# Kernel optimization log

Hardware: AMD Instinct MI355X
Metric: run time of the kernel (lower is better)

## Reference

```python
import jax, jax.numpy as jnp
import numpy as np

B, T, C, H = 2, 2048, 1024, 4
D = C // H
STRIDES = [1, 3, 7, 13]  # spiral_strides[:n_head]
SCALE = 1.0 / float(np.sqrt(D))


def _build_mask():
    """Static [H, T, T] bool mask: spiral positions intersected with causal.
    Replicates: positions = set((i+offset)%T for offset in range(-T//2, T//2, stride)),
    then keep only p <= i."""
    m = np.zeros((H, T, T), dtype=bool)
    i = np.arange(T)
    causal = (np.arange(T)[None, :] <= i[:, None])
    for h in range(H):
        s = STRIDES[h % len(STRIDES)]
        off = np.arange(-(T // 2), T // 2, s)
        pos = (i[:, None] + off[None, :]) % T  # [T, n_off]
        mh = np.zeros((T, T), dtype=bool)
        mh[np.repeat(i, len(off)), pos.ravel()] = True  # set semantics (dupes ok)
        m[h] = mh & causal
    return jnp.asarray(m)

MASK = _build_mask()  # [H, T, T]


def setup_inputs() -> dict:
    ks = jax.random.split(jax.random.key(0), 4)
    s = 0.02
    return {
        "x": jax.random.normal(ks[0], (B, T, C), jnp.float32),
        "Wqk": jax.random.normal(ks[1], (C, C), jnp.float32) * s,
        "bqk": jnp.zeros((C,), jnp.float32),
        "Wv": jax.random.normal(ks[2], (C, C), jnp.float32) * s,
        "bv": jnp.zeros((C,), jnp.float32),
        "Wo": jax.random.normal(ks[3], (C, C), jnp.float32) * s,
        "bo": jnp.zeros((C,), jnp.float32),
    }


def reference(x, Wqk, bqk, Wv, bv, Wo, bo):
    qk = x @ Wqk.T + bqk                                   # [B,T,C]; q == k in source
    q = qk.reshape(B, T, H, D).transpose(0, 2, 1, 3)       # [B,H,T,D]
    v = (x @ Wv.T + bv).reshape(B, T, H, D).transpose(0, 2, 1, 3)
    scores = jnp.einsum('bhid,bhjd->bhij', q, q) * SCALE   # [B,H,T,T]
    NEG = jnp.float32(-1e30)
    logits = jnp.where(MASK[None], scores, NEG)
    w = jax.nn.softmax(logits, axis=-1)
    # Rows with no causal spiral position stay all-zero (matches torch scatter behavior)
    w = jnp.where(MASK[None], w, jnp.float32(0.0))
    out = jnp.einsum('bhij,bhjd->bhid', w, v)              # [B,H,T,D]
    out = out.transpose(0, 2, 1, 3).reshape(B, T, C)
    return out @ Wo.T + bo
```

## Files before the change

### kernel.cpp

```cpp
#include <hip/hip_runtime.h>
#include <cstdint>
#include <cstddef>

typedef unsigned short u16;
typedef uint32_t u32;
typedef __bf16 bf16x8 __attribute__((ext_vector_type(8)));
typedef float f32x4 __attribute__((ext_vector_type(4)));
typedef float f32x16 __attribute__((ext_vector_type(16)));

typedef __attribute__((address_space(1))) void gvoid;
typedef __attribute__((address_space(3))) void lvoid;

__device__ __forceinline__ void g2l16(const void* g, void* l) {
    __builtin_amdgcn_global_load_lds((gvoid*)g, (lvoid*)l, 16, 0, 0);
}

__device__ __forceinline__ u16 f2bf(float f) {
    union { float f; uint32_t u; } v;
    v.f = f;
    uint32_t r = (v.u + 0x7FFFu + ((v.u >> 16) & 1u)) >> 16;
    return (u16)r;
}

__device__ const int T_h[24]  = {0, 1,1,1, 2,2,2,2,2,2,2, 3,3,3,3,3,3,3,3,3,3,3,3,3};
__device__ const int T_g[24]  = {0, 0,1,2, 0,1,2,3,4,5,6, 0,1,2,3,4,5,6,7,8,9,10,11,12};
__device__ const int T_qt[24] = {0, 64,86,108, 130,140,150,160,170,180,190,
                                 200,205,210,215,220,225,230,235,240,245,250,255,260};
__device__ const int T_LQ[24] = {2048, 683,683,682, 293,293,293,293,292,292,292,
                                 158,158,158,158,158,158,158,157,157,157,157,157,157};
__device__ const int T_ktB[24]= {0, 64,86,108, 140,150,160,170,180,190,130,
                                 245,250,255,260,200,205,210,215,220,225,230,235,240};
__device__ const int T_LkB[24]= {2048, 683,683,682, 293,293,293,292,292,292,293,
                                 157,157,157,157,158,158,158,158,158,158,158,157,157};
__device__ const int T_cB[24] = {1, -341,-341,-341, -146,-146,-146,-146,-146,-146,-145,
                                 -79,-79,-79,-79,-78,-78,-78,-78,-78,-78,-78,-78,-78};
__device__ const int T_ktA[24]= {0, 108,64,86, 180,190,130,140,150,160,170,
                                 215,220,225,230,235,240,245,250,255,260,200,205,210};
__device__ const int T_LkA[24]= {0, 682,683,683, 292,292,293,293,293,293,292,
                                 158,158,158,158,157,157,157,157,157,157,158,158,158};
__device__ const int T_cA[24] = {0, -342,-341,-341, -147,-147,-146,-146,-146,-146,-146,
                                 -79,-79,-79,-79,-79,-79,-79,-79,-79,-79,-78,-78,-78};
__device__ const int T_dA[24] = {0, 0,1,1, 0,0,1,1,1,1,1, 0,0,0,0,0,0,0,0,0,0,1,1,1};
__device__ const int T_nc[24] = {16, 6,6,6, 3,3,3,3,3,3,3, 2,2,2,2,2,2,2,2,2,2,2,2,2};

__device__ __forceinline__ void col_geom(int p, int c, int& ntB, int& tA0, int& nt) {
    const int LQ = T_LQ[p];
    const int Mc = c << 7;
    int mmax = Mc + 128; if (mmax > LQ) mmax = LQ; mmax -= 1;
    int jB = mmax + T_cB[p];
    if (jB < 0) jB = 0;
    if (jB > T_LkB[p]) jB = T_LkB[p];
    ntB = (jB + 31) >> 5;
    int jlo = Mc + T_cA[p]; if (jlo < 0) jlo = 0;
    int jhi = mmax + T_dA[p];
    if (jhi > T_LkA[p]) jhi = T_LkA[p];
    tA0 = jlo >> 5;
    int ntA = 0;
    if (jhi > jlo) ntA = ((jhi + 31) >> 5) - tA0;
    nt = ntB + ntA;
}

__device__ __forceinline__ u16* partO_addr(u16* lo, u16* hi, int slot) {
    return (slot < 128) ? (lo + (size_t)slot * 32768) : (hi + (size_t)(slot - 128) * 32768);
}
__device__ __forceinline__ const u16* partO_addr_c(const u16* lo, const u16* hi, int slot) {
    return (slot < 128) ? (lo + (size_t)slot * 32768) : (hi + (size_t)(slot - 128) * 32768);
}

__global__ __launch_bounds__(256)
void cvt_kernel(const float* __restrict__ x, const float* __restrict__ wqk,
                const float* __restrict__ wv, const float* __restrict__ wo,
                u16* __restrict__ out) {
    int i = (blockIdx.x * 256 + threadIdx.x) * 4;
    const float* src;
    int off;
    if (i < 4194304)      { src = x;   off = 0; }
    else if (i < 5242880) { src = wqk; off = 4194304; }
    else if (i < 6291456) { src = wv;  off = 5242880; }
    else                  { src = wo;  off = 6291456; }
    float4 v = *(const float4*)(src + (i - off));
    ushort4 o;
    o.x = f2bf(v.x); o.y = f2bf(v.y); o.z = f2bf(v.z); o.w = f2bf(v.w);
    *(ushort4*)(out + i) = o;
}

__global__ __launch_bounds__(256)
void gemm_qkv(const u16* __restrict__ A, const u16* __restrict__ Bq, const u16* __restrict__ Bv,
              const float* __restrict__ bq, const float* __restrict__ bv,
              u16* __restrict__ qkb, u16* __restrict__ vb) {
    __shared__ __align__(16) u16 As[2][4096], Bqs[2][2048], Bvs[2][2048];
    const int bid = blockIdx.x;
    const int m0 = (bid >> 4) * 128;
    const int n0 = (bid & 15) * 64;
    const int t = threadIdx.x;
    const int lane = t & 63;
    const int wid = t >> 6;
    const int wr = wid >> 1, wc = wid & 1;
    const int l15 = lane & 15, l4 = lane >> 4;

    f32x4 aq[4][2] = {}, av[4][2] = {};

    auto stage = [&](int buf, int kt) {
        const int kbase = kt * 32;
#pragma unroll
        for (int c2 = 0; c2 < 2; ++c2) {
            const int pp = c2 * 4096 + t * 16;
            g2l16(A + (size_t)(m0 + (pp >> 6)) * 1024 + kbase + ((pp & 63) >> 1), (char*)As[buf] + pp);
        }
        const int pb = t * 16;
        const int rb = pb >> 6, kb = (pb & 63) >> 1;
        g2l16(Bq + (size_t)(n0 + rb) * 1024 + kbase + kb, (char*)Bqs[buf] + pb);
        g2l16(Bv + (size_t)(n0 + rb) * 1024 + kbase + kb, (char*)Bvs[buf] + pb);
    };

    stage(0, 0);
    asm volatile("s_waitcnt vmcnt(0)" ::: "memory");
    __syncthreads();

    int cur = 0;
    for (int kt = 0; kt < 32; ++kt) {
        if (kt + 1 < 32) stage(cur ^ 1, kt + 1);
        bf16x8 af[4], bfq[2], bfv[2];
#pragma unroll
        for (int mi = 0; mi < 4; ++mi)
            af[mi] = *(const bf16x8*)((const char*)As[cur] + (wr * 64 + mi * 16 + l15) * 64 + l4 * 16);
#pragma unroll
        for (int ni = 0; ni < 2; ++ni) {
            bfq[ni] = *(const bf16x8*)((const char*)Bqs[cur] + (wc * 32 + ni * 16 + l15) * 64 + l4 * 16);
            bfv[ni] = *(const bf16x8*)((const char*)Bvs[cur] + (wc * 32 + ni * 16 + l15) * 64 + l4 * 16);
        }
#pragma unroll
        for (int mi = 0; mi < 4; ++mi)
#pragma unroll
            for (int ni = 0; ni < 2; ++ni) {
                aq[mi][ni] = __builtin_amdgcn_mfma_f32_16x16x32_bf16(af[mi], bfq[ni], aq[mi][ni], 0, 0, 0);
                av[mi][ni] = __builtin_amdgcn_mfma_f32_16x16x32_bf16(af[mi], bfv[ni], av[mi][ni], 0, 0, 0);
            }
        asm volatile("s_waitcnt vmcnt(0)" ::: "memory");
        __syncthreads();
        cur ^= 1;
    }

    const int mbase = m0 + wr * 64 + l4 * 4;
    const int nbase = n0 + wc * 32 + l15;
#pragma unroll
    for (int ni = 0; ni < 2; ++ni) {
        const int n = nbase + ni * 16;
        const float bq_ = bq[n];
        const float bv_ = bv[n];
#pragma unroll
        for (int mi = 0; mi < 4; ++mi) {
            const int mrow = mbase + mi * 16;
#pragma unroll
            for (int r = 0; r < 4; ++r) {
                qkb[(size_t)(mrow + r) * 1024 + n] = f2bf(aq[mi][ni][r] + bq_);
                vb [(size_t)(mrow + r) * 1024 + n] = f2bf(av[mi][ni][r] + bv_);
            }
        }
    }
}

__device__ __forceinline__ void tile_decode(int tt, int& h, int& cls, int& jt, int& LK) {
    if (tt < 64)       { h = 0; cls = 0;               jt = tt;              LK = 2048; }
    else if (tt < 130) { h = 1; cls = (tt - 64) / 22;  jt = (tt - 64) % 22;  LK = (cls < 2) ? 683 : 682; }
    else if (tt < 200) { h = 2; cls = (tt - 130) / 10; jt = (tt - 130) % 10; LK = (cls < 4) ? 293 : 292; }
    else               { h = 3; cls = (tt - 200) / 5;  jt = (tt - 200) % 5;  LK = (cls < 7) ? 158 : 157; }
}

__global__ __launch_bounds__(256)
void repack_v(const u16* __restrict__ vb, u16* __restrict__ vpack) {
    __shared__ __align__(16) unsigned char sm[16384];
    const int bid = blockIdx.x;
    const int b = bid & 1;
    const int tt = bid >> 1;
    int h, cls, jt, LK;
    tile_decode(tt, h, cls, jt, LK);
    const int s = (h == 0) ? 1 : (h == 1) ? 3 : (h == 2) ? 7 : 13;
    const int j0 = jt * 32;
    int nval = LK - j0; if (nval > 32) nval = 32;
    const int t = threadIdx.x;

#pragma unroll
    for (int i2 = 0; i2 < 4; ++i2) {
        const int p = i2 * 4096 + t * 16;
        const int j = p >> 9;
        const int cb = (p & 511) ^ ((j & 31) << 4);
        const int jj = (j < nval) ? j : (nval - 1);
        const int tok = cls + (j0 + jj) * s;
        g2l16(vb + (size_t)((b * 2048 + tok) * 1024 + h * 256) + (cb >> 1), sm + p);
    }
    asm volatile("s_waitcnt vmcnt(0)" ::: "memory");
    __syncthreads();
    if (nval < 32) {
        const int pb = nval * 512;
        for (int off = pb + t * 16; off < 16384; off += 4096) {
            uint4 z; z.x = 0; z.y = 0; z.z = 0; z.w = 0;
            *(uint4*)(sm + off) = z;
        }
        __syncthreads();
    }
    const size_t tb = (size_t)(b * 265 + tt) * 8192;
#pragma unroll
    for (int i2 = 0; i2 < 4; ++i2) {
        const int o = (i2 * 256 + t) * 8;
        const int slot2 = o >> 9;
        const int idx = (o >> 3) & 63;
        const int jb = (slot2 >> 3) * 16 + (idx >> 5) * 8;
        const int d = (slot2 & 7) * 32 + (idx & 31);
        u32 wpk[4];
#pragma unroll
        for (int e2 = 0; e2 < 4; ++e2) {
            const int j1 = jb + e2 * 2, j2 = j1 + 1;
            const u16 a0 = *(const u16*)(sm + j1 * 512 + (((d >> 3) ^ (j1 & 31)) << 4) + (d & 7) * 2);
            const u16 a1 = *(const u16*)(sm + j2 * 512 + (((d >> 3) ^ (j2 & 31)) << 4) + (d & 7) * 2);
            wpk[e2] = (u32)a0 | ((u32)a1 << 16);
        }
        uint4 pk; pk.x = wpk[0]; pk.y = wpk[1]; pk.z = wpk[2]; pk.w = wpk[3];
        *(uint4*)(vpack + tb + o) = pk;
    }
}

__global__ __launch_bounds__(256)
void repack_k(const u16* __restrict__ qkb, u16* __restrict__ kpack) {
    __shared__ __align__(16) unsigned char sm[16384];
    const int bid = blockIdx.x;
    const int b = bid & 1;
    const int tt = bid >> 1;
    int h, cls, jt, LK;
    tile_decode(tt, h, cls, jt, LK);
    const int s = (h == 0) ? 1 : (h == 1) ? 3 : (h == 2) ? 7 : 13;
    const int j0 = jt * 32;
    int nval = LK - j0; if (nval > 32) nval = 32;
    const int t = threadIdx.x;

#pragma unroll
    for (int i2 = 0; i2 < 4; ++i2) {
        const int p = i2 * 4096 + t * 16;
        const int j = p >> 9;
        const int cb = (p & 511) ^ ((j & 31) << 4);
        const int jj = (j < nval) ? j : (nval - 1);
        const int tok = cls + (j0 + jj) * s;
        g2l16(qkb + (size_t)((b * 2048 + tok) * 1024 + h * 256) + (cb >> 1), sm + p);
    }
    asm volatile("s_waitcnt vmcnt(0)" ::: "memory");
    __syncthreads();
    const size_t tb = (size_t)(b * 265 + tt) * 8192;
#pragma unroll
    for (int i2 = 0; i2 < 4; ++i2) {
        const int o = (i2 * 256 + t) * 8;
        const int dc = o >> 9;
        const int idx = (o >> 3) & 63;
        const int j = idx & 31;
        const int d0 = dc * 16 + (idx >> 5) * 8;
        const uint4 pk = *(const uint4*)(sm + j * 512 + ((d0 * 2) ^ ((j & 31) << 4)));
        *(uint4*)(kpack + tb + o) = pk;
    }
}

__global__ __launch_bounds__(256, 2)
void attn_kernel(const u16* __restrict__ kpack, const u16* __restrict__ vpack,
                 u16* __restrict__ attnb, u16* __restrict__ partLo, u16* __restrict__ partHi,
                 float* __restrict__ mlbuf) {
    __shared__ __align__(16) unsigned char sm[65536];
    static constexpr int CGc[24] = {0,16,22,28,34,37,40,43,46,49,52,55,
                                    57,59,61,63,65,67,69,71,73,75,77,79};
    static constexpr int EXc[24] = {0,56,64,72,80,82,84,86,88,90,92,94,
                                    94,94,94,94,94,94,94,94,94,94,94,94};
    static constexpr int Tpc[24] = {72,14,14,14,5,5,5,5,5,5,5,2,2,2,2,2,2,2,2,2,2,2,2,2};

    const int bid = blockIdx.x;
    const int xcd = bid & 7, slot = bid >> 3;
    const int b = xcd & 1, quad = xcd >> 1;
    int hsel, hcb;
    if (quad <= 1) {
        if (slot < 36)      { hsel = 0; hcb = quad * 36 + slot; }
        else if (slot < 49) { hsel = 3; hcb = quad * 13 + (slot - 36); }
        else return;
    } else if (quad == 2) {
        if (slot >= 42) return;
        hsel = 1; hcb = slot;
    } else {
        if (slot >= 35) return;
        hsel = 2; hcb = slot;
    }
    int p = (hsel == 0) ? 0 : (hsel == 1) ? 1 : (hsel == 2) ? 4 : 11;
    int rb = hcb;
    while (rb >= Tpc[p]) { rb -= Tpc[p]; ++p; }
    int colg = CGc[p], exb = EXc[p];

    const int LQ = T_LQ[p];
    const int cB = T_cB[p], cA = T_cA[p], dA = T_dA[p];
    const int LKB = T_LkB[p], LKA = T_LkA[p];
    const int ktB = T_ktB[p], ktA = T_ktA[p];
    const int h = T_h[p], g = T_g[p], nc = T_nc[p], qt0 = T_qt[p];
    const int s = (h == 0) ? 1 : (h == 1) ? 3 : (h == 2) ? 7 : 13;

    int col = 0, chunk = 0, ntB = 0, tA0 = 0, nt = 0;
    for (int c = nc - 1; c >= 0; --c) {
        const int Mc = c << 7;
        int mmax = Mc + 128; if (mmax > LQ) mmax = LQ; mmax -= 1;
        int jB = mmax + cB; if (jB < 0) jB = 0; if (jB > LKB) jB = LKB;
        const int nb = (jB + 31) >> 5;
        int jlo = Mc + cA; if (jlo < 0) jlo = 0;
        int jhi = mmax + dA; if (jhi > LKA) jhi = LKA;
        const int ta = jlo >> 5;
        const int na = (jhi > jlo) ? (((jhi + 31) >> 5) - ta) : 0;
        const int n = nb + na;
        const int nch2 = (n + 7) >> 3;
        if (rb < nch2) { col = c; chunk = rb; ntB = nb; tA0 = ta; nt = n; break; }
        rb -= nch2; ++colg; exb += nch2 - 1;
    }
    const int nch = (nt + 7) >> 3;
    const int PBi = b * 265;

    const int t = threadIdx.x;
    const int w = t >> 6;
    const int l = t & 63;
    const int l31 = l & 31, h5 = l >> 5;
    const int m = (col << 7) + (w << 5) + l31;
    const float c2 = 0.09016844f;
    const int lane16 = l * 16;

    bf16x8 qf[16];
    {
        const u16* qb = kpack + (size_t)(PBi + qt0 + col * 4 + w) * 8192 + l * 8;
#pragma unroll
        for (int dc = 0; dc < 16; ++dc)
            qf[dc] = *(const bf16x8*)(qb + dc * 512);
    }

    auto tileof = [&](int tv) -> int {
        return (tv < ntB) ? (ktB + tv) : (ktA + tA0 + (tv - ntB));
    };
    auto stage = [&](int tv, int buf) {
        const size_t tb = (size_t)(PBi + tileof(tv)) * 8192;
        unsigned char* Kd = sm + buf * 32768;
        unsigned char* Vd = Kd + 16384;
#pragma unroll
        for (int i2 = 0; i2 < 4; ++i2) {
            const int off = i2 * 4096 + t * 16;
            g2l16(kpack + tb + (off >> 1), Kd + off);
            g2l16(vpack + tb + (off >> 1), Vd + off);
        }
    };

    const int tt0 = chunk * 8;
    int tt1 = tt0 + 8; if (tt1 > nt) tt1 = nt;

    f32x16 o[8] = {};
    float mrun = -3.0e38f, lrun = 0.0f;

    stage(tt0, 0);
    asm volatile("s_waitcnt vmcnt(0)" ::: "memory");
    __syncthreads();

    int buf = 0;
    for (int tv = tt0; tv < tt1; ++tv) {
        if (tv + 1 < tt1) stage(tv + 1, buf ^ 1);

        int j0, lo, hi;
        if (tv < ntB) { j0 = tv << 5; lo = -100000; hi = cB; }
        else { const int ta = tA0 + tv - ntB; j0 = ta << 5; lo = cA; hi = dA; }

        const unsigned char* Kb = sm + buf * 32768;
        const unsigned char* Vb = Kb + 16384;

        f32x16 sacc = {};
#pragma unroll
        for (int dc = 0; dc < 16; ++dc) {
            const bf16x8 kf = *(const bf16x8*)(Kb + dc * 1024 + lane16);
            sacc = __builtin_amdgcn_mfma_f32_32x32x16_bf16(kf, qf[dc], sacc, 0, 0, 0);
        }

        const int ebase = j0 - m;
        float tmax = -3.0e38f;
#pragma unroll
        for (int r = 0; r < 16; ++r) {
            const int km = (r & 3) + 8 * (r >> 2) + 4 * h5;
            const int e = ebase + km;
            const bool ok = (e >= lo) && (e < hi);
            sacc[r] = ok ? sacc[r] : -3.0e38f;
            tmax = fmaxf(tmax, sacc[r]);
        }
        tmax = fmaxf(tmax, __shfl_xor(tmax, 32, 64));
        if (!__all(tmax <= mrun + 8.0f)) {
            const float mnew = fmaxf(mrun, tmax);
            const float fsc = __builtin_amdgcn_exp2f((mrun - mnew) * c2);
            lrun *= fsc;
#pragma unroll
            for (int ch = 0; ch < 8; ++ch)
#pragma unroll
                for (int r = 0; r < 16; ++r)
                    o[ch][r] *= fsc;
            mrun = mnew;
        }
        float psum = 0.0f;
#pragma unroll
        for (int r = 0; r < 16; ++r) {
            const float pv = (sacc[r] > -1.0e37f) ? __builtin_amdgcn_exp2f((sacc[r] - mrun) * c2) : 0.0f;
            sacc[r] = pv;
            psum += pv;
        }
        lrun += psum;

        uint32_t w0, w1, w2, w3, w4, w5, w6, w7;
        asm("v_cvt_pk_bf16_f32 %0,%1,%2" : "=v"(w0) : "v"(sacc[0]),  "v"(sacc[1]));
        asm("v_cvt_pk_bf16_f32 %0,%1,%2" : "=v"(w1) : "v"(sacc[2]),  "v"(sacc[3]));
        asm("v_cvt_pk_bf16_f32 %0,%1,%2" : "=v"(w2) : "v"(sacc[4]),  "v"(sacc[5]));
        asm("v_cvt_pk_bf16_f32 %0,%1,%2" : "=v"(w3) : "v"(sacc[6]),  "v"(sacc[7]));
        asm("v_cvt_pk_bf16_f32 %0,%1,%2" : "=v"(w4) : "v"(sacc[8]),  "v"(sacc[9]));
        asm("v_cvt_pk_bf16_f32 %0,%1,%2" : "=v"(w5) : "v"(sacc[10]), "v"(sacc[11]));
        asm("v_cvt_pk_bf16_f32 %0,%1,%2" : "=v"(w6) : "v"(sacc[12]), "v"(sacc[13]));
        asm("v_cvt_pk_bf16_f32 %0,%1,%2" : "=v"(w7) : "v"(sacc[14]), "v"(sacc[15]));
        asm("v_permlane32_swap_b32 %0, %1" : "+v"(w0), "+v"(w2));
        asm("v_permlane32_swap_b32 %0, %1" : "+v"(w1), "+v"(w3));
        asm("v_permlane32_swap_b32 %0, %1" : "+v"(w4), "+v"(w6));
        asm("v_permlane32_swap_b32 %0, %1" : "+v"(w5), "+v"(w7));
        union { uint32_t u[4]; bf16x8 v; } p0u, p1u;
        p0u.u[0] = w0; p0u.u[1] = w1; p0u.u[2] = w2; p0u.u[3] = w3;
        p1u.u[0] = w4; p1u.u[1] = w5; p1u.u[2] = w6; p1u.u[3] = w7;

#pragma unroll
        for (int kk = 0; kk < 2; ++kk) {
            const bf16x8 pf = kk ? p1u.v : p0u.v;
#pragma unroll
            for (int ch = 0; ch < 8; ++ch) {
                const bf16x8 vf = *(const bf16x8*)(Vb + (kk * 8 + ch) * 1024 + lane16);
                o[ch] = __builtin_amdgcn_mfma_f32_32x32x16_bf16(vf, pf, o[ch], 0, 0, 0);
            }
        }

        asm volatile("s_waitcnt vmcnt(0)" ::: "memory");
        __syncthreads();
        buf ^= 1;
    }

    lrun += __shfl_xor(lrun, 32, 64);

    float scale = 1.0f;
    u16* ab;
    const int qm = (w << 5) + l31;
    if (nch == 1) {
        scale = (lrun > 0.0f) ? 1.0f / lrun : 0.0f;
        ab = attnb + ((size_t)(b * 2048 + g + m * s)) * 1024 + h * 256;
    } else {
        if (h5 == 0 && m < LQ) {
            const int colid = b * 81 + colg;
            mlbuf[(size_t)((colid * 8 + chunk) * 256) + qm * 2]     = mrun;
            mlbuf[(size_t)((colid * 8 + chunk) * 256) + qm * 2 + 1] = lrun;
        }
        if (chunk == 0)
            ab = attnb + ((size_t)(b * 2048 + g + m * s)) * 1024 + h * 256;
        else
            ab = partO_addr(partLo, partHi, b * 94 + exb + chunk - 1) + (size_t)qm * 256;
    }

    if (m < LQ) {
#pragma unroll
        for (int ch = 0; ch < 8; ++ch) {
#pragma unroll
            for (int g2 = 0; g2 < 4; ++g2) {
                ushort4 wv4;
                wv4.x = f2bf(o[ch][g2 * 4 + 0] * scale);
                wv4.y = f2bf(o[ch][g2 * 4 + 1] * scale);
                wv4.z = f2bf(o[ch][g2 * 4 + 2] * scale);
                wv4.w = f2bf(o[ch][g2 * 4 + 3] * scale);
                *(ushort4*)(ab + ch * 32 + 8 * g2 + 4 * h5) = wv4;
            }
        }
    }
}

__global__ __launch_bounds__(256)
void combine_kernel(const u16* __restrict__ partLo, const u16* __restrict__ partHi,
                    const float* __restrict__ mlbuf, u16* __restrict__ attnb) {
    static constexpr int MCc[24] = {0,14,18,22,26,28,30,32,34,36,38,40,
                                    40,40,40,40,40,40,40,40,40,40,40,40};
    static constexpr int CGc[24] = {0,16,22,28,34,37,40,43,46,49,52,55,
                                    57,59,61,63,65,67,69,71,73,75,77,79};
    static constexpr int EXc[24] = {0,56,64,72,80,82,84,86,88,90,92,94,
                                    94,94,94,94,94,94,94,94,94,94,94,94};
    const int b = blockIdx.x & 1;
    int rb = blockIdx.x >> 1;
    int p = 0, base = 0, colg = 0, exb = 0;
#pragma unroll
    for (int i = 1; i < 24; ++i)
        if (rb >= MCc[i]) { p = i; base = MCc[i]; colg = CGc[i]; exb = EXc[i]; }
    rb -= base;

    int col = 0, nch = 0;
    for (int c = T_nc[p] - 1; c >= 0; --c) {
        int nb, ta, n;
        col_geom(p, c, nb, ta, n);
        const int nc2 = (n + 7) >> 3;
        if (nc2 > 1) {
            if (rb == 0) { col = c; nch = nc2; break; }
            --rb;
        }
        ++colg; exb += nc2 - 1;
    }
    const int h = T_h[p], g = T_g[p];
    const int s = (h == 0) ? 1 : (h == 1) ? 3 : (h == 2) ? 7 : 13;
    const int LQ = T_LQ[p];
    const int colid = b * 81 + colg;
    const float c2 = 0.09016844f;

    const int t = threadIdx.x;
    const int q = t >> 1, dpart = (t & 1) * 128;
    const int m = (col << 7) + q;

    float mj[8], lj[8];
#pragma unroll
    for (int j5 = 0; j5 < 8; ++j5) {
        if (j5 < nch) {
            mj[j5] = mlbuf[(size_t)((colid * 8 + j5) * 256) + q * 2];
            lj[j5] = mlbuf[(size_t)((colid * 8 + j5) * 256) + q * 2 + 1];
        } else { mj[j5] = -3.0e38f; lj[j5] = 0.0f; }
    }
    float M = -3.0e38f;
#pragma unroll
    for (int j5 = 0; j5 < 8; ++j5) if (j5 < nch) M = fmaxf(M, mj[j5]);
    float L = 0.0f, al[8];
#pragma unroll
    for (int j5 = 0; j5 < 8; ++j5) {
        al[j5] = (j5 < nch) ? __builtin_amdgcn_exp2f((mj[j5] - M) * c2) : 0.0f;
        L += lj[j5] * al[j5];
    }
    const float inv = (L > 0.0f) ? 1.0f / L : 0.0f;
#pragma unroll
    for (int j5 = 0; j5 < 8; ++j5) al[j5] *= inv;

    u16* dst = attnb + ((size_t)(b * 2048 + g + m * s)) * 1024 + h * 256 + dpart;

    for (int ss = 0; ss < 4; ++ss) {
        float acc32[32];
#pragma unroll
        for (int e = 0; e < 32; ++e) acc32[e] = 0.0f;
#pragma unroll
        for (int j5 = 0; j5 < 8; ++j5) {
            if (j5 >= nch) continue;
            const u16* src = (j5 == 0)
                ? (dst + ss * 32)
                : (partO_addr_c(partLo, partHi, b * 94 + exb + j5 - 1) + (size_t)q * 256 + dpart + ss * 32);
            const float sc = al[j5];
#pragma unroll
            for (int w4 = 0; w4 < 4; ++w4) {
                const uint4 pk = *(const uint4*)(src + w4 * 8);
                const u32 ww[4] = { pk.x, pk.y, pk.z, pk.w };
#pragma unroll
                for (int e = 0; e < 4; ++e) {
                    union { u32 u; float f; } lo2, hi2;
                    lo2.u = ww[e] << 16;
                    hi2.u = ww[e] & 0xffff0000u;
                    acc32[w4 * 8 + e * 2]     += sc * lo2.f;
                    acc32[w4 * 8 + e * 2 + 1] += sc * hi2.f;
                }
            }
        }
        if (m < LQ) {
#pragma unroll
            for (int w4 = 0; w4 < 4; ++w4) {
                uint4 pk;
                pk.x = (u32)f2bf(acc32[w4 * 8 + 0]) | ((u32)f2bf(acc32[w4 * 8 + 1]) << 16);
                pk.y = (u32)f2bf(acc32[w4 * 8 + 2]) | ((u32)f2bf(acc32[w4 * 8 + 3]) << 16);
                pk.z = (u32)f2bf(acc32[w4 * 8 + 4]) | ((u32)f2bf(acc32[w4 * 8 + 5]) << 16);
                pk.w = (u32)f2bf(acc32[w4 * 8 + 6]) | ((u32)f2bf(acc32[w4 * 8 + 7]) << 16);
                *(uint4*)(dst + ss * 32 + w4 * 8) = pk;
            }
        }
    }
}

__global__ __launch_bounds__(256)
void gemm_out(const u16* __restrict__ A, const u16* __restrict__ Bw,
              const float* __restrict__ bias, float* __restrict__ outp) {
    __shared__ __align__(16) u16 As[2][4096], Bs[2][2048];
    const int bid = blockIdx.x;
    const int m0 = (bid >> 4) * 128;
    const int n0 = (bid & 15) * 64;
    const int t = threadIdx.x;
    const int lane = t & 63;
    const int wid = t >> 6;
    const int wr = wid >> 1, wc = wid & 1;
    const int l15 = lane & 15, l4 = lane >> 4;

    f32x4 acc[4][2] = {};

    auto stage = [&](int buf, int kt) {
        const int kbase = kt * 32;
#pragma unroll
        for (int c2 = 0; c2 < 2; ++c2) {
            const int pp = c2 * 4096 + t * 16;
            g2l16(A + (size_t)(m0 + (pp >> 6)) * 1024 + kbase + ((pp & 63) >> 1), (char*)As[buf] + pp);
        }
        const int pb = t * 16;
        g2l16(Bw + (size_t)(n0 + (pb >> 6)) * 1024 + kbase + ((pb & 63) >> 1), (char*)Bs[buf] + pb);
    };

    stage(0, 0);
    asm volatile("s_waitcnt vmcnt(0)" ::: "memory");
    __syncthreads();

    int cur = 0;
    for (int kt = 0; kt < 32; ++kt) {
        if (kt + 1 < 32) stage(cur ^ 1, kt + 1);
        bf16x8 af[4], bfr[2];
#pragma unroll
        for (int mi = 0; mi < 4; ++mi)
            af[mi] = *(const bf16x8*)((const char*)As[cur] + (wr * 64 + mi * 16 + l15) * 64 + l4 * 16);
#pragma unroll
        for (int ni = 0; ni < 2; ++ni)
            bfr[ni] = *(const bf16x8*)((const char*)Bs[cur] + (wc * 32 + ni * 16 + l15) * 64 + l4 * 16);
#pragma unroll
        for (int mi = 0; mi < 4; ++mi)
#pragma unroll
            for (int ni = 0; ni < 2; ++ni)
                acc[mi][ni] = __builtin_amdgcn_mfma_f32_16x16x32_bf16(af[mi], bfr[ni], acc[mi][ni], 0, 0, 0);
        asm volatile("s_waitcnt vmcnt(0)" ::: "memory");
        __syncthreads();
        cur ^= 1;
    }

    const int mbase = m0 + wr * 64 + l4 * 4;
    const int nbase = n0 + wc * 32 + l15;
#pragma unroll
    for (int ni = 0; ni < 2; ++ni) {
        const int n = nbase + ni * 16;
        const float bv = bias[n];
#pragma unroll
        for (int mi = 0; mi < 4; ++mi) {
            const int mrow = mbase + mi * 16;
#pragma unroll
            for (int r = 0; r < 4; ++r)
                outp[(size_t)(mrow + r) * 1024 + n] = acc[mi][ni][r] + bv;
        }
    }
}

extern "C" void kernel_launch(void* const* d_in, const int* in_sizes, int n_in,
                              void* d_out, int out_size, void* d_ws, size_t ws_size,
                              hipStream_t stream) {
    const float* x   = (const float*)d_in[0];
    const float* Wqk = (const float*)d_in[1];
    const float* bqk = (const float*)d_in[2];
    const float* Wv  = (const float*)d_in[3];
    const float* bv  = (const float*)d_in[4];
    const float* Wo  = (const float*)d_in[5];
    const float* bo  = (const float*)d_in[6];
    float* out = (float*)d_out;

    u16* ws     = (u16*)d_ws;
    u16* xb     = ws;
    u16* wqkb   = ws + 4194304;
    u16* wvb    = ws + 5242880;
    u16* wob    = ws + 6291456;
    u16* qkb    = ws + 7340032;
    u16* vb     = ws + 11534336;
    u16* kpack  = ws + 11534336;
    u16* vpack  = ws + 15876096;
    u16* attnb  = ws;
    u16* partLo = ws + 7340032;
    u16* partHi = ws + 4194304;
    float* mlbuf = (float*)d_out;

    cvt_kernel<<<7168, 256, 0, stream>>>(x, Wqk, Wv, Wo, ws);
    gemm_qkv<<<512, 256, 0, stream>>>(xb, wqkb, wvb, bqk, bv, qkb, vb);
    repack_v<<<530, 256, 0, stream>>>(vb, vpack);
    repack_k<<<530, 256, 0, stream>>>(qkb, kpack);
    attn_kernel<<<392, 256, 0, stream>>>(kpack, vpack, attnb, partLo, partHi, mlbuf);
    combine_kernel<<<80, 256, 0, stream>>>(partLo, partHi, mlbuf, attnb);
    gemm_out<<<512, 256, 0, stream>>>(attnb, wob, bo, out);
}
```

Before: 132.7 us.

## Fuse K/V repack kernels and add MFMA priority hints and occupancy bounds

Merges the separate repack_v and repack_k kernels into one repack_kv launch that gathers both K and V tiles into a 32KB LDS buffer, removing a kernel launch and a duplicate index computation. Because kpack previously aliased the vb buffer, it moves kpack and vpack to new workspace offsets, which needs a larger workspace. It also wraps the MFMA loops in the GEMMs and the attention kernel with s_setprio raises, and adds a min-blocks-per-CU hint of 3 to both GEMMs, which may constrain register allocation.

New measurement: 123.5 us. -6.9%, faster.

```diff
diff --git a/kernel.cpp b/kernel.cpp
--- a/kernel.cpp
+++ b/kernel.cpp
@@ -84,7 +84,7 @@
     *(ushort4*)(out + i) = o;
 }
 
-__global__ __launch_bounds__(256)
+__global__ __launch_bounds__(256, 3)
 void gemm_qkv(const u16* __restrict__ A, const u16* __restrict__ Bq, const u16* __restrict__ Bv,
               const float* __restrict__ bq, const float* __restrict__ bv,
               u16* __restrict__ qkb, u16* __restrict__ vb) {
@@ -129,6 +129,7 @@
             bfq[ni] = *(const bf16x8*)((const char*)Bqs[cur] + (wc * 32 + ni * 16 + l15) * 64 + l4 * 16);
             bfv[ni] = *(const bf16x8*)((const char*)Bvs[cur] + (wc * 32 + ni * 16 + l15) * 64 + l4 * 16);
         }
+        __builtin_amdgcn_s_setprio(1);
 #pragma unroll
         for (int mi = 0; mi < 4; ++mi)
 #pragma unroll
@@ -136,6 +137,7 @@
                 aq[mi][ni] = __builtin_amdgcn_mfma_f32_16x16x32_bf16(af[mi], bfq[ni], aq[mi][ni], 0, 0, 0);
                 av[mi][ni] = __builtin_amdgcn_mfma_f32_16x16x32_bf16(af[mi], bfv[ni], av[mi][ni], 0, 0, 0);
             }
+        __builtin_amdgcn_s_setprio(0);
         asm volatile("s_waitcnt vmcnt(0)" ::: "memory");
         __syncthreads();
         cur ^= 1;
@@ -168,8 +170,9 @@
 }
 
 __global__ __launch_bounds__(256)
-void repack_v(const u16* __restrict__ vb, u16* __restrict__ vpack) {
-    __shared__ __align__(16) unsigned char sm[16384];
+void repack_kv(const u16* __restrict__ qkb, const u16* __restrict__ vb,
+               u16* __restrict__ kpack, u16* __restrict__ vpack) {
+    __shared__ __align__(16) unsigned char sm[32768];
     const int bid = blockIdx.x;
     const int b = bid & 1;
     const int tt = bid >> 1;
@@ -186,64 +189,20 @@
         const int j = p >> 9;
         const int cb = (p & 511) ^ ((j & 31) << 4);
         const int jj = (j < nval) ? j : (nval - 1);
-        const int tok = cls + (j0 + jj) * s;
-        g2l16(vb + (size_t)((b * 2048 + tok) * 1024 + h * 256) + (cb >> 1), sm + p);
+        const size_t gofs = (size_t)((b * 2048 + cls + (j0 + jj) * s) * 1024 + h * 256) + (cb >> 1);
+        g2l16(qkb + gofs, sm + p);
+        g2l16(vb  + gofs, sm + 16384 + p);
     }
     asm volatile("s_waitcnt vmcnt(0)" ::: "memory");
     __syncthreads();
     if (nval < 32) {
-        const int pb = nval * 512;
-        for (int off = pb + t * 16; off < 16384; off += 4096) {
+        const int pb = 16384 + nval * 512;
+        for (int off = pb + t * 16; off < 32768; off += 4096) {
             uint4 z; z.x = 0; z.y = 0; z.z = 0; z.w = 0;
             *(uint4*)(sm + off) = z;
         }
         __syncthreads();
     }
-    const size_t tb = (size_t)(b * 265 + tt) * 8192;
-#pragma unroll
-    for (int i2 = 0; i2 < 4; ++i2) {
-        const int o = (i2 * 256 + t) * 8;
-        const int slot2 = o >> 9;
-        const int idx = (o >> 3) & 63;
-        const int jb = (slot2 >> 3) * 16 + (idx >> 5) * 8;
-        const int d = (slot2 & 7) * 32 + (idx & 31);
-        u32 wpk[4];
-#pragma unroll
-        for (int e2 = 0; e2 < 4; ++e2) {
-            const int j1 = jb + e2 * 2, j2 = j1 + 1;
-            const u16 a0 = *(const u16*)(sm + j1 * 512 + (((d >> 3) ^ (j1 & 31)) << 4) + (d & 7) * 2);
-            const u16 a1 = *(const u16*)(sm + j2 * 512 + (((d >> 3) ^ (j2 & 31)) << 4) + (d & 7) * 2);
-            wpk[e2] = (u32)a0 | ((u32)a1 << 16);
-        }
-        uint4 pk; pk.x = wpk[0]; pk.y = wpk[1]; pk.z = wpk[2]; pk.w = wpk[3];
-        *(uint4*)(vpack + tb + o) = pk;
-    }
-}
-
-__global__ __launch_bounds__(256)
-void repack_k(const u16* __restrict__ qkb, u16* __restrict__ kpack) {
-    __shared__ __align__(16) unsigned char sm[16384];
-    const int bid = blockIdx.x;
-    const int b = bid & 1;
-    const int tt = bid >> 1;
-    int h, cls, jt, LK;
-    tile_decode(tt, h, cls, jt, LK);
-    const int s = (h == 0) ? 1 : (h == 1) ? 3 : (h == 2) ? 7 : 13;
-    const int j0 = jt * 32;
-    int nval = LK - j0; if (nval > 32) nval = 32;
-    const int t = threadIdx.x;
-
-#pragma unroll
-    for (int i2 = 0; i2 < 4; ++i2) {
-        const int p = i2 * 4096 + t * 16;
-        const int j = p >> 9;
-        const int cb = (p & 511) ^ ((j & 31) << 4);
-        const int jj = (j < nval) ? j : (nval - 1);
-        const int tok = cls + (j0 + jj) * s;
-        g2l16(qkb + (size_t)((b * 2048 + tok) * 1024 + h * 256) + (cb >> 1), sm + p);
-    }
-    asm volatile("s_waitcnt vmcnt(0)" ::: "memory");
-    __syncthreads();
     const size_t tb = (size_t)(b * 265 + tt) * 8192;
 #pragma unroll
     for (int i2 = 0; i2 < 4; ++i2) {
@@ -254,6 +213,24 @@
         const int d0 = dc * 16 + (idx >> 5) * 8;
         const uint4 pk = *(const uint4*)(sm + j * 512 + ((d0 * 2) ^ ((j & 31) << 4)));
         *(uint4*)(kpack + tb + o) = pk;
+    }
+#pragma unroll
+    for (int i2 = 0; i2 < 4; ++i2) {
+        const int o = (i2 * 256 + t) * 8;
+        const int slot2 = o >> 9;
+        const int idx = (o >> 3) & 63;
+        const int jb = (slot2 >> 3) * 16 + (idx >> 5) * 8;
+        const int d = (slot2 & 7) * 32 + (idx & 31);
+        u32 wpk[4];
+#pragma unroll
+        for (int e2 = 0; e2 < 4; ++e2) {
+            const int j1 = jb + e2 * 2, j2 = j1 + 1;
+            const u16 a0 = *(const u16*)(sm + 16384 + j1 * 512 + (((d >> 3) ^ (j1 & 31)) << 4) + (d & 7) * 2);
+            const u16 a1 = *(const u16*)(sm + 16384 + j2 * 512 + (((d >> 3) ^ (j2 & 31)) << 4) + (d & 7) * 2);
+            wpk[e2] = (u32)a0 | ((u32)a1 << 16);
+        }
+        uint4 pk; pk.x = wpk[0]; pk.y = wpk[1]; pk.z = wpk[2]; pk.w = wpk[3];
+        *(uint4*)(vpack + tb + o) = pk;
     }
 }
 
@@ -366,11 +343,13 @@
         const unsigned char* Vb = Kb + 16384;
 
         f32x16 sacc = {};
+        __builtin_amdgcn_s_setprio(1);
 #pragma unroll
         for (int dc = 0; dc < 16; ++dc) {
             const bf16x8 kf = *(const bf16x8*)(Kb + dc * 1024 + lane16);
             sacc = __builtin_amdgcn_mfma_f32_32x32x16_bf16(kf, qf[dc], sacc, 0, 0, 0);
         }
+        __builtin_amdgcn_s_setprio(0);
 
         const int ebase = j0 - m;
         float tmax = -3.0e38f;
@@ -420,6 +399,7 @@
         p0u.u[0] = w0; p0u.u[1] = w1; p0u.u[2] = w2; p0u.u[3] = w3;
         p1u.u[0] = w4; p1u.u[1] = w5; p1u.u[2] = w6; p1u.u[3] = w7;
 
+        __builtin_amdgcn_s_setprio(1);
 #pragma unroll
         for (int kk = 0; kk < 2; ++kk) {
             const bf16x8 pf = kk ? p1u.v : p0u.v;
@@ -429,6 +409,7 @@
                 o[ch] = __builtin_amdgcn_mfma_f32_32x32x16_bf16(vf, pf, o[ch], 0, 0, 0);
             }
         }
+        __builtin_amdgcn_s_setprio(0);
 
         asm volatile("s_waitcnt vmcnt(0)" ::: "memory");
         __syncthreads();
@@ -571,7 +552,7 @@
     }
 }
 
-__global__ __launch_bounds__(256)
+__global__ __launch_bounds__(256, 3)
 void gemm_out(const u16* __restrict__ A, const u16* __restrict__ Bw,
               const float* __restrict__ bias, float* __restrict__ outp) {
     __shared__ __align__(16) u16 As[2][4096], Bs[2][2048];
@@ -611,11 +592,13 @@
 #pragma unroll
         for (int ni = 0; ni < 2; ++ni)
             bfr[ni] = *(const bf16x8*)((const char*)Bs[cur] + (wc * 32 + ni * 16 + l15) * 64 + l4 * 16);
+        __builtin_amdgcn_s_setprio(1);
 #pragma unroll
         for (int mi = 0; mi < 4; ++mi)
 #pragma unroll
             for (int ni = 0; ni < 2; ++ni)
                 acc[mi][ni] = __builtin_amdgcn_mfma_f32_16x16x32_bf16(af[mi], bfr[ni], acc[mi][ni], 0, 0, 0);
+        __builtin_amdgcn_s_setprio(0);
         asm volatile("s_waitcnt vmcnt(0)" ::: "memory");
         __syncthreads();
         cur ^= 1;
@@ -656,8 +639,8 @@
     u16* wob    = ws + 6291456;
     u16* qkb    = ws + 7340032;
     u16* vb     = ws + 11534336;
-    u16* kpack  = ws + 11534336;
-    u16* vpack  = ws + 15876096;
+    u16* kpack  = ws + 15728640;
+    u16* vpack  = ws + 20070400;
     u16* attnb  = ws;
     u16* partLo = ws + 7340032;
     u16* partHi = ws + 4194304;
@@ -665,8 +648,7 @@
 
     cvt_kernel<<<7168, 256, 0, stream>>>(x, Wqk, Wv, Wo, ws);
     gemm_qkv<<<512, 256, 0, stream>>>(xb, wqkb, wvb, bqk, bv, qkb, vb);
-    repack_v<<<530, 256, 0, stream>>>(vb, vpack);
-    repack_k<<<530, 256, 0, stream>>>(qkb, kpack);
+    repack_kv<<<530, 256, 0, stream>>>(qkb, vb, kpack, vpack);
     attn_kernel<<<392, 256, 0, stream>>>(kpack, vpack, attnb, partLo, partHi, mlbuf);
     combine_kernel<<<80, 256, 0, stream>>>(partLo, partHi, mlbuf, attnb);
     gemm_out<<<512, 256, 0, stream>>>(attnb, wob, bo, out);
```
